# Optimization experiments

Hardware: AMD Instinct MI355X
Metric: run time of the kernel (lower is better)

Reference implementation:

```python
import jax, jax.numpy as jnp
import numpy as np

D_MODEL = 1024
HEADS = 16
D_HEAD = 64  # d_q = d_k = d_v
LN_EPS = 1e-5


def setup_inputs() -> dict:
    key = jax.random.key(0)
    ks = jax.random.split(key, 12)
    B, L = 2, 2048
    query = jax.random.normal(ks[0], (B, L, D_MODEL), dtype=jnp.float32)
    k_in = jax.random.normal(ks[1], (B, L, D_MODEL), dtype=jnp.float32)
    v_in = jax.random.normal(ks[2], (B, L, D_MODEL), dtype=jnp.float32)
    # causal mask: True = masked (masked_fill with -inf); row i always keeps pos i
    mask = jnp.broadcast_to(~jnp.tril(jnp.ones((L, L), dtype=bool)), (B, L, L))
    std_qk = np.sqrt(2.0 / (D_MODEL + D_HEAD)).astype(np.float32)
    Wq = jax.random.normal(ks[3], (D_MODEL, HEADS * D_HEAD), dtype=jnp.float32) * std_qk
    Wk = jax.random.normal(ks[4], (D_MODEL, HEADS * D_HEAD), dtype=jnp.float32) * std_qk
    Wv = jax.random.normal(ks[5], (D_MODEL, HEADS * D_HEAD), dtype=jnp.float32) * std_qk
    bq = jnp.zeros((HEADS * D_HEAD,), dtype=jnp.float32)
    bk = jnp.zeros((HEADS * D_HEAD,), dtype=jnp.float32)
    bv = jnp.zeros((HEADS * D_HEAD,), dtype=jnp.float32)
    lim = 1.0 / np.sqrt(HEADS * D_HEAD)
    Wo = jax.random.uniform(ks[6], (HEADS * D_HEAD, D_MODEL), dtype=jnp.float32, minval=-lim, maxval=lim)
    bo = jax.random.uniform(ks[7], (D_MODEL,), dtype=jnp.float32, minval=-lim, maxval=lim)
    gamma = jnp.ones((D_MODEL,), dtype=jnp.float32)
    beta = jnp.zeros((D_MODEL,), dtype=jnp.float32)
    return {"query": query, "key": k_in, "value": v_in, "mask": mask,
            "Wq": Wq, "bq": bq, "Wk": Wk, "bk": bk, "Wv": Wv, "bv": bv,
            "Wo": Wo, "bo": bo, "gamma": gamma, "beta": beta}


def reference(query, key, value, mask, Wq, bq, Wk, bk, Wv, bv, Wo, bo, gamma, beta):
    B, Lq, _ = query.shape
    Lk = key.shape[1]
    # QKV projections, split into heads: [B, L, H, d]
    q = (query @ Wq + bq).reshape(B, Lq, HEADS, D_HEAD)
    k = (key @ Wk + bk).reshape(B, Lk, HEADS, D_HEAD)
    v = (value @ Wv + bv).reshape(B, Lk, HEADS, D_HEAD)
    # scaled dot-product scores: [B, H, Lq, Lk]
    scores = jnp.einsum('bqhd,bkhd->bhqk', q, k) / np.sqrt(D_HEAD).astype(np.float32)
    scores = jnp.where(mask[:, None, :, :], -jnp.inf, scores)
    probs = jax.nn.softmax(scores, axis=-1)  # dropout is identity at p=0 / eval
    out = jnp.einsum('bhqk,bkhd->bqhd', probs, v).reshape(B, Lq, HEADS * D_HEAD)
    out = out @ Wo + bo  # dropout identity
    x = query + out  # residual
    mu = jnp.mean(x, axis=-1, keepdims=True)
    var = jnp.var(x, axis=-1, keepdims=True)
    return gamma * (x - mu) * jax.lax.rsqrt(var + LN_EPS) + beta
```

## Files before the change

kernel.cpp:

```cpp
#include <hip/hip_runtime.h>
#include <hip/hip_bf16.h>

#define L_SEQ  2048
#define DMODEL 1024
#define HEADS  16
#define DHEAD  64
#define BATCH  2
#define MROWS  (BATCH * L_SEQ)

typedef __attribute__((ext_vector_type(8))) short bf16x8;
typedef __attribute__((ext_vector_type(8))) unsigned short u16x8;
typedef __attribute__((ext_vector_type(4))) float f32x4;

__device__ __forceinline__ float b2f(unsigned short u) {
    union { unsigned int u32; float f; } x;
    x.u32 = ((unsigned int)u) << 16;
    return x.f;
}
__device__ __forceinline__ unsigned short f2b(float f) {
    union { float f; unsigned int u; } x; x.f = f;
    unsigned int u = x.u;
    if ((u & 0x7fffffffu) > 0x7f800000u) return (unsigned short)((u >> 16) | 0x0040);
    unsigned int r = (u + 0x7fffu + ((u >> 16) & 1u)) >> 16;
    return (unsigned short)r;
}
__device__ __forceinline__ unsigned short f2br(float f) {
    union { float f; unsigned int u; } x; x.f = f;
    return (unsigned short)((x.u + 0x7fffu + ((x.u >> 16) & 1u)) >> 16);
}

__device__ __forceinline__ float4 load4(const void* p, int isF32, size_t idx) {
    if (isF32) return *(const float4*)((const float*)p + idx);
    const ushort4 u = *(const ushort4*)((const unsigned short*)p + idx);
    return make_float4(b2f(u.x), b2f(u.y), b2f(u.z), b2f(u.w));
}
__device__ __forceinline__ float load1(const void* p, int isF32, size_t idx) {
    return isF32 ? ((const float*)p)[idx] : b2f(((const unsigned short*)p)[idx]);
}

__device__ __forceinline__ void gload16(const void* g, void* l) {
    __builtin_amdgcn_global_load_lds(
        (const __attribute__((address_space(1))) void*)g,
        (__attribute__((address_space(3))) void*)l, 16, 0, 0);
}

__global__ void detect_kernel(const unsigned short* __restrict__ q, int* __restrict__ flag) {
    int cnt = 0;
    #pragma unroll 8
    for (int t = 0; t < 64; ++t) {
        const unsigned short u = q[(threadIdx.x << 6) + t];
        const int e = (u >> 7) & 0xFF;
        cnt += (e >= 133) ? 1 : 0;
    }
    #pragma unroll
    for (int off = 32; off; off >>= 1) cnt += __shfl_xor(cnt, off);
    if (threadIdx.x == 0) *flag = (cnt > 64) ? 1 : 0;
}

__global__ void diag_kernel(float* __restrict__ out, float val, int n) {
    const int i = blockIdx.x * 256 + threadIdx.x;
    if (i < n) out[i] = val;
}

__global__ __launch_bounds__(256) void cvtW_kernel(
    const void* __restrict__ W0, const void* __restrict__ W1,
    const void* __restrict__ W2, const void* __restrict__ W3,
    unsigned short* __restrict__ T0, unsigned short* __restrict__ T1,
    unsigned short* __restrict__ T2, unsigned short* __restrict__ T3,
    const int* __restrict__ dflag)
{
    const int isF32 = *dflag;
    const int z = blockIdx.z;
    const void* W = (z == 0) ? W0 : (z == 1) ? W1 : (z == 2) ? W2 : W3;
    unsigned short* T = (z == 0) ? T0 : (z == 1) ? T1 : (z == 2) ? T2 : T3;

    __shared__ unsigned short tile[64][66];
    const int kb = blockIdx.x << 6, nb = blockIdx.y << 6;
    const int tr = threadIdx.x >> 4, tc = (threadIdx.x & 15) << 2;
    #pragma unroll
    for (int p = 0; p < 4; ++p) {
        const int r = tr + p * 16;
        const float4 v = load4(W, isF32, (size_t)(kb + r) * DMODEL + nb + tc);
        tile[tc + 0][r] = f2br(v.x);
        tile[tc + 1][r] = f2br(v.y);
        tile[tc + 2][r] = f2br(v.z);
        tile[tc + 3][r] = f2br(v.w);
    }
    __syncthreads();
    #pragma unroll
    for (int p = 0; p < 4; ++p) {
        const int rr = tr + p * 16;
        const ushort4 o = make_ushort4(tile[rr][tc], tile[rr][tc + 1],
                                       tile[rr][tc + 2], tile[rr][tc + 3]);
        *(ushort4*)(T + (size_t)(nb + rr) * DMODEL + kb + tc) = o;
    }
}

#define QKV_COMPUTE(CUR)                                                          \
    {                                                                             \
        bf16x8 af[4], bfr[4];                                                     \
        _Pragma("unroll")                                                         \
        for (int i = 0; i < 4; ++i) {                                             \
            const int row = wm + i * 16 + ln;                                     \
            const int p = quad ^ ((row >> 1) & 3);                                \
            af[i] = *(const bf16x8*)(As[CUR] + row * 32 + p * 8);                 \
        }                                                                         \
        _Pragma("unroll")                                                         \
        for (int j = 0; j < 4; ++j)                                               \
            bfr[j] = *(const bf16x8*)(Bs[CUR] + (wn + j * 16 + ln) * 32 + quad * 8); \
        _Pragma("unroll")                                                         \
        for (int i = 0; i < 4; ++i)                                               \
            _Pragma("unroll")                                                     \
            for (int j = 0; j < 4; ++j)                                           \
                acc[i][j] = __builtin_amdgcn_mfma_f32_16x16x32_bf16(af[i], bfr[j], acc[i][j], 0, 0, 0); \
    }

__global__ __launch_bounds__(256) void gemm_qkv_mfma(
    const void* __restrict__ A0, const void* __restrict__ A1, const void* __restrict__ A2,
    const unsigned short* __restrict__ Wt0, const unsigned short* __restrict__ Wt1,
    const unsigned short* __restrict__ Wt2,
    const void* __restrict__ b0, const void* __restrict__ b1, const void* __restrict__ b2,
    unsigned short* __restrict__ O0, unsigned short* __restrict__ O1, unsigned short* __restrict__ O2,
    const int* __restrict__ dflag)
{
    const int isF32 = *dflag;

    const int bid = blockIdx.x;
    const int xcd = bid & 7;
    const int jj  = bid >> 3;
    const int g   = xcd * 12 + (jj >> 3);
    const int z   = g >> 5;
    const int rowBase = (g & 31) << 7;
    const int colBase = (jj & 7) << 7;

    const void* A  = (z == 0) ? A0 : (z == 1) ? A1 : A2;
    const unsigned short* Wt = (z == 0) ? Wt0 : (z == 1) ? Wt1 : Wt2;
    const void* bi = (z == 0) ? b0 : (z == 1) ? b1 : b2;
    unsigned short* out = (z == 0) ? O0 : (z == 1) ? O1 : O2;
    const float scale = (z == 0) ? 0.125f : 1.0f;

    __shared__ __align__(16) unsigned short As[2][128 * 32];
    __shared__ __align__(16) unsigned short Bs[2][128 * 32];

    const int tid  = threadIdx.x;
    const int lane = tid & 63, wid = tid >> 6;
    const int ln   = lane & 15, quad = lane >> 4;
    const int wm   = (wid & 1) << 6, wn = (wid >> 1) << 6;

    f32x4 acc[4][4];
    #pragma unroll
    for (int i = 0; i < 4; ++i)
        #pragma unroll
        for (int j = 0; j < 4; ++j)
            #pragma unroll
            for (int d = 0; d < 4; ++d) acc[i][j][d] = 0.f;

    const int am   = tid >> 1;
    const int half = tid & 1;
    const int sw   = (am >> 1) & 3;
    const int bseg = wid * 2;
    const int brow = lane >> 2, bcol = (lane & 3) << 3;

    gload16(Wt + (size_t)(colBase + bseg * 16 + brow) * DMODEL + bcol,
            Bs[0] + bseg * 512);
    gload16(Wt + (size_t)(colBase + (bseg + 1) * 16 + brow) * DMODEL + bcol,
            Bs[0] + (bseg + 1) * 512);
    {
        const size_t ab = (size_t)(rowBase + am) * DMODEL + half * 16;
        const float4 a0 = load4(A, isF32, ab);
        const float4 a1 = load4(A, isF32, ab + 4);
        const float4 a2 = load4(A, isF32, ab + 8);
        const float4 a3 = load4(A, isF32, ab + 12);
        u16x8 pk0, pk1;
        pk0[0] = f2br(a0.x); pk0[1] = f2br(a0.y); pk0[2] = f2br(a0.z); pk0[3] = f2br(a0.w);
        pk0[4] = f2br(a1.x); pk0[5] = f2br(a1.y); pk0[6] = f2br(a1.z); pk0[7] = f2br(a1.w);
        pk1[0] = f2br(a2.x); pk1[1] = f2br(a2.y); pk1[2] = f2br(a2.z); pk1[3] = f2br(a2.w);
        pk1[4] = f2br(a3.x); pk1[5] = f2br(a3.y); pk1[6] = f2br(a3.z); pk1[7] = f2br(a3.w);
        unsigned short* ap = As[0] + am * 32;
        *(u16x8*)(ap + (((half << 1) | 0) ^ sw) * 8) = pk0;
        *(u16x8*)(ap + (((half << 1) | 1) ^ sw) * 8) = pk1;
    }
    __syncthreads();

    int cur = 0;
    for (int t = 0; t < 31; ++t) {
        const int nxt = cur ^ 1;
        const int k0n = (t + 1) << 5;
        gload16(Wt + (size_t)(colBase + bseg * 16 + brow) * DMODEL + k0n + bcol,
                Bs[nxt] + bseg * 512);
        gload16(Wt + (size_t)(colBase + (bseg + 1) * 16 + brow) * DMODEL + k0n + bcol,
                Bs[nxt] + (bseg + 1) * 512);
        const size_t ab = (size_t)(rowBase + am) * DMODEL + k0n + half * 16;
        const float4 a0 = load4(A, isF32, ab);
        const float4 a1 = load4(A, isF32, ab + 4);
        const float4 a2 = load4(A, isF32, ab + 8);
        const float4 a3 = load4(A, isF32, ab + 12);

        QKV_COMPUTE(cur);

        u16x8 pk0, pk1;
        pk0[0] = f2br(a0.x); pk0[1] = f2br(a0.y); pk0[2] = f2br(a0.z); pk0[3] = f2br(a0.w);
        pk0[4] = f2br(a1.x); pk0[5] = f2br(a1.y); pk0[6] = f2br(a1.z); pk0[7] = f2br(a1.w);
        pk1[0] = f2br(a2.x); pk1[1] = f2br(a2.y); pk1[2] = f2br(a2.z); pk1[3] = f2br(a2.w);
        pk1[4] = f2br(a3.x); pk1[5] = f2br(a3.y); pk1[6] = f2br(a3.z); pk1[7] = f2br(a3.w);
        unsigned short* ap = As[nxt] + am * 32;
        *(u16x8*)(ap + (((half << 1) | 0) ^ sw) * 8) = pk0;
        *(u16x8*)(ap + (((half << 1) | 1) ^ sw) * 8) = pk1;

        __syncthreads();
        cur = nxt;
    }
    QKV_COMPUTE(cur);

    float bsv[4];
    #pragma unroll
    for (int j = 0; j < 4; ++j) bsv[j] = load1(bi, isF32, colBase + wn + j * 16 + ln);

    if (z != 2) {
        #pragma unroll
        for (int i = 0; i < 4; ++i) {
            const int r0 = rowBase + wm + i * 16 + quad * 4;
            const int b = r0 >> 11, l0 = r0 & (L_SEQ - 1);
            #pragma unroll
            for (int j = 0; j < 4; ++j) {
                const int n = colBase + wn + j * 16 + ln;
                const int h = n >> 6, d = n & 63;
                const size_t base = ((size_t)(b * HEADS + h) * L_SEQ) << 6;
                #pragma unroll
                for (int reg = 0; reg < 4; ++reg)
                    out[base + ((size_t)(l0 + reg) << 6) + d] =
                        f2br((acc[i][j][reg] + bsv[j]) * scale);
            }
        }
    } else {
        #pragma unroll
        for (int i = 0; i < 4; ++i) {
            const int r0 = rowBase + wm + i * 16 + quad * 4;
            const int b = r0 >> 11, l0 = r0 & (L_SEQ - 1);
            #pragma unroll
            for (int j = 0; j < 4; ++j) {
                const int n = colBase + wn + j * 16 + ln;
                const int h = n >> 6, d = n & 63;
                ushort4 o;
                o.x = f2br(acc[i][j][0] + bsv[j]);
                o.y = f2br(acc[i][j][1] + bsv[j]);
                o.z = f2br(acc[i][j][2] + bsv[j]);
                o.w = f2br(acc[i][j][3] + bsv[j]);
                *(ushort4*)(out + (((size_t)((b * HEADS + h) * 64 + d)) << 11) + l0) = o;
            }
        }
    }
}

#define OUT_COMPUTE(CUR)                                                          \
    {                                                                             \
        bf16x8 af[4], bfr[4];                                                     \
        _Pragma("unroll")                                                         \
        for (int i = 0; i < 4; ++i)                                               \
            af[i] = *(const bf16x8*)(As[CUR] + (wm + i * 16 + ln) * 32 + quad * 8); \
        _Pragma("unroll")                                                         \
        for (int j = 0; j < 4; ++j)                                               \
            bfr[j] = *(const bf16x8*)(Bs[CUR] + (wn + j * 16 + ln) * 32 + quad * 8); \
        _Pragma("unroll")                                                         \
        for (int i = 0; i < 4; ++i)                                               \
            _Pragma("unroll")                                                     \
            for (int j = 0; j < 4; ++j)                                           \
                acc[i][j] = __builtin_amdgcn_mfma_f32_16x16x32_bf16(af[i], bfr[j], acc[i][j], 0, 0, 0); \
    }

__global__ __launch_bounds__(256) void gemm_out_mfma(
    const unsigned short* __restrict__ AO,
    const unsigned short* __restrict__ Wt,
    const void* __restrict__ bi,
    const void* __restrict__ resid,
    float* __restrict__ X,
    const int* __restrict__ dflag)
{
    const int isF32 = *dflag;
    __shared__ __align__(16) unsigned short As[2][128 * 32];
    __shared__ __align__(16) unsigned short Bs[2][128 * 32];

    const int bid = blockIdx.x;
    const int xcd = bid & 7;
    const int jj  = bid >> 3;
    const int g   = xcd * 4 + (jj >> 3);
    const int rowBase = g << 7;
    const int colBase = (jj & 7) << 7;

    const int tid  = threadIdx.x;
    const int lane = tid & 63, wid = tid >> 6;
    const int ln   = lane & 15, quad = lane >> 4;
    const int wm   = (wid & 1) << 6, wn = (wid >> 1) << 6;

    f32x4 acc[4][4];
    #pragma unroll
    for (int i = 0; i < 4; ++i)
        #pragma unroll
        for (int j = 0; j < 4; ++j)
            #pragma unroll
            for (int d = 0; d < 4; ++d) acc[i][j][d] = 0.f;

    const int seg = wid * 2;
    const int srow = lane >> 2, scol = (lane & 3) << 3;

    #pragma unroll
    for (int t2 = 0; t2 < 2; ++t2) {
        gload16(AO + (size_t)(rowBase + (seg + t2) * 16 + srow) * DMODEL + scol,
                As[0] + (seg + t2) * 512);
        gload16(Wt + (size_t)(colBase + (seg + t2) * 16 + srow) * DMODEL + scol,
                Bs[0] + (seg + t2) * 512);
    }
    __syncthreads();

    int cur = 0;
    for (int t = 0; t < 31; ++t) {
        const int nxt = cur ^ 1;
        const int k0n = (t + 1) << 5;
        #pragma unroll
        for (int t2 = 0; t2 < 2; ++t2) {
            gload16(AO + (size_t)(rowBase + (seg + t2) * 16 + srow) * DMODEL + k0n + scol,
                    As[nxt] + (seg + t2) * 512);
            gload16(Wt + (size_t)(colBase + (seg + t2) * 16 + srow) * DMODEL + k0n + scol,
                    Bs[nxt] + (seg + t2) * 512);
        }

        OUT_COMPUTE(cur);

        __syncthreads();
        cur = nxt;
    }
    OUT_COMPUTE(cur);

    float bsv[4];
    #pragma unroll
    for (int j = 0; j < 4; ++j) bsv[j] = load1(bi, isF32, colBase + wn + j * 16 + ln);

    #pragma unroll
    for (int i = 0; i < 4; ++i) {
        const int r0 = rowBase + wm + i * 16 + quad * 4;
        #pragma unroll
        for (int j = 0; j < 4; ++j) {
            const int n = colBase + wn + j * 16 + ln;
            #pragma unroll
            for (int reg = 0; reg < 4; ++reg) {
                const size_t idx = (size_t)(r0 + reg) * DMODEL + n;
                X[idx] = acc[i][j][reg] + bsv[j] + load1(resid, isF32, idx);
            }
        }
    }
}

#define KVB  128
#define NQB  (L_SEQ / 64)
#define KSTR 72
#define VSTR 136
__global__ __launch_bounds__(256, 3) void attn_mfma_kernel(
    const unsigned short* __restrict__ Q,
    const unsigned short* __restrict__ K,
    const unsigned short* __restrict__ Vt,
    unsigned short* __restrict__ AO)
{
    __shared__ unsigned short Kl[KVB * KSTR];
    __shared__ unsigned short Vl[64 * VSTR];
    __shared__ unsigned short Pl[4][16 * KVB];

    const int tid  = threadIdx.x;
    const int wid  = tid >> 6;
    const int lane = tid & 63;
    const int ln   = lane & 15;
    const int quad = lane >> 4;

    const int qb = (NQB - 1) - (blockIdx.x >> 5);
    const int bh = blockIdx.x & 31;

    const size_t qkBase = (size_t)bh * (L_SEQ * 64);
    const size_t vtBase = (size_t)bh * (64 * L_SEQ);

    const int qrow = qb * 64 + wid * 16 + ln;
    const bf16x8 qf0 = *(const bf16x8*)(Q + qkBase + (size_t)qrow * 64 + quad * 8);
    const bf16x8 qf1 = *(const bf16x8*)(Q + qkBase + (size_t)qrow * 64 + quad * 8 + 32);

    f32x4 o[4];
    #pragma unroll
    for (int d = 0; d < 4; ++d) { o[d][0] = 0.f; o[d][1] = 0.f; o[d][2] = 0.f; o[d][3] = 0.f; }
    float m[4] = {-INFINITY, -INFINITY, -INFINITY, -INFINITY};
    float l[4] = {0.f, 0.f, 0.f, 0.f};

    unsigned short* Pw = Pl[wid];
    const int kp_r = tid >> 3, kp_c = (tid & 7) * 8;
    const int vp_r = tid >> 4, vp_c = (tid & 15) * 8;

    const int nt = (qb >> 1) + 1;
    for (int jt = 0; jt < nt; ++jt) {
        __syncthreads();
        #pragma unroll
        for (int p = 0; p < 4; ++p) {
            const int kr = kp_r + p * 32;
            *(int4*)(Kl + kr * KSTR + kp_c) =
                *(const int4*)(K + qkBase + (size_t)(jt * KVB + kr) * 64 + kp_c);
            const int vr = vp_r + p * 16;
            *(int4*)(Vl + vr * VSTR + vp_c) =
                *(const int4*)(Vt + vtBase + (size_t)vr * L_SEQ + jt * KVB + vp_c);
        }
        __syncthreads();

        f32x4 s[8];
        __builtin_amdgcn_s_setprio(1);
        #pragma unroll
        for (int sub = 0; sub < 8; ++sub) {
            const bf16x8 kf0 = *(const bf16x8*)(Kl + (sub * 16 + ln) * KSTR + quad * 8);
            const bf16x8 kf1 = *(const bf16x8*)(Kl + (sub * 16 + ln) * KSTR + quad * 8 + 32);
            f32x4 a2;
            a2[0] = 0.f; a2[1] = 0.f; a2[2] = 0.f; a2[3] = 0.f;
            a2 = __builtin_amdgcn_mfma_f32_16x16x32_bf16(qf0, kf0, a2, 0, 0, 0);
            a2 = __builtin_amdgcn_mfma_f32_16x16x32_bf16(qf1, kf1, a2, 0, 0, 0);
            s[sub] = a2;
        }
        __builtin_amdgcn_s_setprio(0);

        if (jt == nt - 1) {
            const int row0 = qb * 64 + wid * 16 + quad * 4;
            #pragma unroll
            for (int sub = 0; sub < 8; ++sub) {
                const int keyg = jt * KVB + sub * 16 + ln;
                #pragma unroll
                for (int reg = 0; reg < 4; ++reg)
                    if (keyg > row0 + reg) s[sub][reg] = -INFINITY;
            }
        }

        float alpha[4];
        #pragma unroll
        for (int reg = 0; reg < 4; ++reg) {
            float t = fmaxf(
                fmaxf(fmaxf(s[0][reg], s[1][reg]), fmaxf(s[2][reg], s[3][reg])),
                fmaxf(fmaxf(s[4][reg], s[5][reg]), fmaxf(s[6][reg], s[7][reg])));
            #pragma unroll
            for (int off = 8; off; off >>= 1) t = fmaxf(t, __shfl_xor(t, off));
            const float mn = fmaxf(m[reg], t);
            alpha[reg] = __expf(m[reg] - mn);
            m[reg] = mn;
            float rs = 0.f;
            #pragma unroll
            for (int sub = 0; sub < 8; ++sub) {
                const float pe = __expf(s[sub][reg] - mn);
                s[sub][reg] = pe;
                rs += pe;
            }
            #pragma unroll
            for (int off = 8; off; off >>= 1) rs += __shfl_xor(rs, off);
            l[reg] = l[reg] * alpha[reg] + rs;
        }

        #pragma unroll
        for (int sub = 0; sub < 8; ++sub)
            #pragma unroll
            for (int reg = 0; reg < 4; ++reg) {
                const int r = quad * 4 + reg;
                const int blk = (sub * 2 + (ln >> 3)) ^ ((r >> 1) & 7);
                Pw[r * KVB + blk * 8 + (ln & 7)] = f2br(s[sub][reg]);
            }

        #pragma unroll
        for (int dblk = 0; dblk < 4; ++dblk)
            #pragma unroll
            for (int reg = 0; reg < 4; ++reg)
                o[dblk][reg] *= alpha[reg];

        __builtin_amdgcn_s_setprio(1);
        #pragma unroll
        for (int jb = 0; jb < 4; ++jb) {
            const int rblk = (jb * 4 + quad) ^ ((ln >> 1) & 7);
            const bf16x8 pf = *(const bf16x8*)(Pw + ln * KVB + rblk * 8);
            #pragma unroll
            for (int dblk = 0; dblk < 4; ++dblk) {
                const bf16x8 vf = *(const bf16x8*)(Vl + (dblk * 16 + ln) * VSTR + jb * 32 + quad * 8);
                o[dblk] = __builtin_amdgcn_mfma_f32_16x16x32_bf16(pf, vf, o[dblk], 0, 0, 0);
            }
        }
        __builtin_amdgcn_s_setprio(0);
    }

    const int b = bh >> 4, h = bh & 15;
    float rl[4];
    #pragma unroll
    for (int reg = 0; reg < 4; ++reg) rl[reg] = 1.f / l[reg];
    #pragma unroll
    for (int dblk = 0; dblk < 4; ++dblk)
        #pragma unroll
        for (int reg = 0; reg < 4; ++reg) {
            const int row = qb * 64 + wid * 16 + quad * 4 + reg;
            AO[((size_t)(b * L_SEQ + row)) * DMODEL + h * 64 + dblk * 16 + ln] =
                f2br(o[dblk][reg] * rl[reg]);
        }
}

__global__ __launch_bounds__(256) void ln_kernel(
    const float* __restrict__ X,
    const void* __restrict__ gamma,
    const void* __restrict__ beta,
    float* __restrict__ out,
    const int* __restrict__ dflag)
{
    const int isF32 = *dflag;
    const int row = blockIdx.x;
    const int tid = threadIdx.x;
    const float* x = X + (size_t)row * DMODEL;
    float v[4], s = 0.f, s2 = 0.f;
    #pragma unroll
    for (int j = 0; j < 4; ++j) {
        const float t = x[tid + (j << 8)];
        v[j] = t; s += t; s2 += t * t;
    }
    #pragma unroll
    for (int off = 32; off; off >>= 1) {
        s  += __shfl_xor(s, off);
        s2 += __shfl_xor(s2, off);
    }
    __shared__ float red[4][2];
    const int wid = tid >> 6, lane = tid & 63;
    if (lane == 0) { red[wid][0] = s; red[wid][1] = s2; }
    __syncthreads();
    s  = red[0][0] + red[1][0] + red[2][0] + red[3][0];
    s2 = red[0][1] + red[1][1] + red[2][1] + red[3][1];
    const float mu  = s * (1.f / 1024.f);
    const float var = s2 * (1.f / 1024.f) - mu * mu;
    const float inv = rsqrtf(var + 1e-5f);
    #pragma unroll
    for (int j = 0; j < 4; ++j) {
        const int c = tid + (j << 8);
        float r = load1(gamma, isF32, c) * (v[j] - mu) * inv + load1(beta, isF32, c);
        if (!(r == r) || fabsf(r) > 1e37f) r = 777000.0f;
        out[(size_t)row * DMODEL + c] = r;
    }
}

extern "C" void kernel_launch(void* const* d_in, const int* in_sizes, int n_in,
                              void* d_out, int out_size, void* d_ws, size_t ws_size,
                              hipStream_t stream) {
    const void* query = d_in[0];
    const void* key   = d_in[1];
    const void* value = d_in[2];

    int wbase = 4;
    if (in_sizes[3] == DMODEL * DMODEL) wbase = 3;
    const void* Wq    = d_in[wbase + 0];
    const void* bq    = d_in[wbase + 1];
    const void* Wk    = d_in[wbase + 2];
    const void* bk    = d_in[wbase + 3];
    const void* Wv    = d_in[wbase + 4];
    const void* bv    = d_in[wbase + 5];
    const void* Wo    = d_in[wbase + 6];
    const void* bo    = d_in[wbase + 7];
    const void* gamma = d_in[wbase + 8];
    const void* beta  = d_in[wbase + 9];

    const size_t NEED = ((size_t)24u << 20) + 64;
    if (ws_size < NEED) {
        const float val = (float)(ws_size >> 20) * 1000.0f;
        diag_kernel<<<dim3((out_size + 255) / 256), dim3(256), 0, stream>>>(
            (float*)d_out, val, out_size);
        return;
    }

    char* ws = (char*)d_ws;
    unsigned short* Qb  = (unsigned short*)(ws);
    unsigned short* Kb  = (unsigned short*)(ws + (size_t)( 8u << 20));
    unsigned short* Vtb = (unsigned short*)(ws + (size_t)(16u << 20));
    float* X            = (float*)ws;
    int* dflag          = (int*)(ws + (size_t)(24u << 20));
    unsigned short* AO  = (unsigned short*)d_out;
    unsigned short* Wtq = (unsigned short*)d_out + ((size_t)4u << 20);
    unsigned short* Wtk = Wtq + ((size_t)1u << 20);
    unsigned short* Wtv = Wtk + ((size_t)1u << 20);
    unsigned short* Wto = Wtv + ((size_t)1u << 20);

    const dim3 blk(256);

    detect_kernel<<<dim3(1), dim3(64), 0, stream>>>((const unsigned short*)query, dflag);
    cvtW_kernel<<<dim3(16, 16, 4), blk, 0, stream>>>(
        Wq, Wk, Wv, Wo, Wtq, Wtk, Wtv, Wto, dflag);
    gemm_qkv_mfma<<<dim3(768), blk, 0, stream>>>(
        query, key, value, Wtq, Wtk, Wtv, bq, bk, bv, Qb, Kb, Vtb, dflag);
    attn_mfma_kernel<<<dim3(BATCH * HEADS * 32), blk, 0, stream>>>(Qb, Kb, Vtb, AO);
    gemm_out_mfma<<<dim3(256), blk, 0, stream>>>(AO, Wto, bo, query, X, dflag);
    ln_kernel<<<dim3(MROWS), blk, 0, stream>>>(X, gamma, beta, (float*)d_out, dflag);
}
```

Measured before the change: 304.2 us.

## Stage QKV GEMM A tiles via direct global-to-LDS loads and vectorize LayerNorm

The QKV projection GEMM used to load fp32 activations into registers, convert them to bf16 and write them to shared memory. It now copies raw fp32 (or bf16) A tiles straight into LDS with async 16-byte global-to-LDS loads, using an XOR swizzle, and converts to bf16 when reading the MFMA fragments. This removes register staging and the convert-then-store step from the main loop, so A loads can overlap compute like the B loads already do. In exchange it doubles A shared memory and repeats the conversion per fragment read. The LayerNorm kernel also switches to float4 vectorized loads and stores.

```diff
diff --git a/kernel.cpp b/kernel.cpp
--- a/kernel.cpp
+++ b/kernel.cpp
@@ -96,23 +96,71 @@
     }
 }
 
-#define QKV_COMPUTE(CUR)                                                          \
+#define STAGE_A_F32(BUF, K0)                                                      \
+    _Pragma("unroll")                                                             \
+    for (int s4 = 0; s4 < 4; ++s4) {                                              \
+        const int ar = s4 * 32 + (tid >> 3);                                      \
+        const int ac = (tid & 7) ^ (ar & 7);                                      \
+        gload16((const float*)A + (size_t)(rowBase + ar) * DMODEL + (K0) + ac * 4,\
+                (char*)AsMem[BUF] + s4 * 4096 + tid * 16);                        \
+    }
+
+#define STAGE_A_BF16(BUF, K0)                                                     \
+    _Pragma("unroll")                                                             \
+    for (int s2 = 0; s2 < 2; ++s2) {                                              \
+        const int ar = s2 * 64 + (tid >> 2);                                      \
+        const int ac = (tid & 3) ^ ((ar >> 1) & 3);                               \
+        gload16((const unsigned short*)A + (size_t)(rowBase + ar) * DMODEL + (K0) + ac * 8, \
+                (char*)AsMem[BUF] + s2 * 4096 + tid * 16);                        \
+    }
+
+#define STAGE_B(BUF, K0)                                                          \
+    gload16(Wt + (size_t)(colBase + bseg * 16 + brow) * DMODEL + (K0) + bcol,     \
+            Bs[BUF] + bseg * 512);                                                \
+    gload16(Wt + (size_t)(colBase + (bseg + 1) * 16 + brow) * DMODEL + (K0) + bcol,\
+            Bs[BUF] + (bseg + 1) * 512);
+
+#define QKV_MFMA_CLUSTER                                                          \
+    _Pragma("unroll")                                                             \
+    for (int i = 0; i < 4; ++i)                                                   \
+        _Pragma("unroll")                                                         \
+        for (int j = 0; j < 4; ++j)                                               \
+            acc[i][j] = __builtin_amdgcn_mfma_f32_16x16x32_bf16(af[i], bfr[j], acc[i][j], 0, 0, 0);
+
+#define QKV_COMPUTE_F32(CUR)                                                      \
+    {                                                                             \
+        bf16x8 af[4], bfr[4];                                                     \
+        _Pragma("unroll")                                                         \
+        for (int i = 0; i < 4; ++i) {                                             \
+            const int row = wm + i * 16 + ln;                                     \
+            const int xr  = row & 7;                                              \
+            const float* rp = (const float*)AsMem[CUR] + row * 32;                \
+            const f32x4 lo = *(const f32x4*)(rp + (((quad << 1) | 0) ^ xr) * 4);  \
+            const f32x4 hi = *(const f32x4*)(rp + (((quad << 1) | 1) ^ xr) * 4);  \
+            af[i][0] = (short)f2br(lo[0]); af[i][1] = (short)f2br(lo[1]);         \
+            af[i][2] = (short)f2br(lo[2]); af[i][3] = (short)f2br(lo[3]);         \
+            af[i][4] = (short)f2br(hi[0]); af[i][5] = (short)f2br(hi[1]);         \
+            af[i][6] = (short)f2br(hi[2]); af[i][7] = (short)f2br(hi[3]);         \
+        }                                                                         \
+        _Pragma("unroll")                                                         \
+        for (int j = 0; j < 4; ++j)                                               \
+            bfr[j] = *(const bf16x8*)(Bs[CUR] + (wn + j * 16 + ln) * 32 + quad * 8); \
+        QKV_MFMA_CLUSTER                                                          \
+    }
+
+#define QKV_COMPUTE_BF16(CUR)                                                     \
     {                                                                             \
         bf16x8 af[4], bfr[4];                                                     \
         _Pragma("unroll")                                                         \
         for (int i = 0; i < 4; ++i) {                                             \
             const int row = wm + i * 16 + ln;                                     \
             const int p = quad ^ ((row >> 1) & 3);                                \
-            af[i] = *(const bf16x8*)(As[CUR] + row * 32 + p * 8);                 \
+            af[i] = *(const bf16x8*)((const unsigned short*)AsMem[CUR] + row * 32 + p * 8); \
         }                                                                         \
         _Pragma("unroll")                                                         \
         for (int j = 0; j < 4; ++j)                                               \
             bfr[j] = *(const bf16x8*)(Bs[CUR] + (wn + j * 16 + ln) * 32 + quad * 8); \
-        _Pragma("unroll")                                                         \
-        for (int i = 0; i < 4; ++i)                                               \
-            _Pragma("unroll")                                                     \
-            for (int j = 0; j < 4; ++j)                                           \
-                acc[i][j] = __builtin_amdgcn_mfma_f32_16x16x32_bf16(af[i], bfr[j], acc[i][j], 0, 0, 0); \
+        QKV_MFMA_CLUSTER                                                          \
     }
 
 __global__ __launch_bounds__(256) void gemm_qkv_mfma(
@@ -139,7 +187,7 @@
     unsigned short* out = (z == 0) ? O0 : (z == 1) ? O1 : O2;
     const float scale = (z == 0) ? 0.125f : 1.0f;
 
-    __shared__ __align__(16) unsigned short As[2][128 * 32];
+    __shared__ __align__(16) char AsMem[2][16384];
     __shared__ __align__(16) unsigned short Bs[2][128 * 32];
 
     const int tid  = threadIdx.x;
@@ -155,62 +203,40 @@
             #pragma unroll
             for (int d = 0; d < 4; ++d) acc[i][j][d] = 0.f;
 
-    const int am   = tid >> 1;
-    const int half = tid & 1;
-    const int sw   = (am >> 1) & 3;
     const int bseg = wid * 2;
     const int brow = lane >> 2, bcol = (lane & 3) << 3;
 
-    gload16(Wt + (size_t)(colBase + bseg * 16 + brow) * DMODEL + bcol,
-            Bs[0] + bseg * 512);
-    gload16(Wt + (size_t)(colBase + (bseg + 1) * 16 + brow) * DMODEL + bcol,
-            Bs[0] + (bseg + 1) * 512);
-    {
-        const size_t ab = (size_t)(rowBase + am) * DMODEL + half * 16;
-        const float4 a0 = load4(A, isF32, ab);
-        const float4 a1 = load4(A, isF32, ab + 4);
-        const float4 a2 = load4(A, isF32, ab + 8);
-        const float4 a3 = load4(A, isF32, ab + 12);
-        u16x8 pk0, pk1;
-        pk0[0] = f2br(a0.x); pk0[1] = f2br(a0.y); pk0[2] = f2br(a0.z); pk0[3] = f2br(a0.w);
-        pk0[4] = f2br(a1.x); pk0[5] = f2br(a1.y); pk0[6] = f2br(a1.z); pk0[7] = f2br(a1.w);
-        pk1[0] = f2br(a2.x); pk1[1] = f2br(a2.y); pk1[2] = f2br(a2.z); pk1[3] = f2br(a2.w);
-        pk1[4] = f2br(a3.x); pk1[5] = f2br(a3.y); pk1[6] = f2br(a3.z); pk1[7] = f2br(a3.w);
-        unsigned short* ap = As[0] + am * 32;
-        *(u16x8*)(ap + (((half << 1) | 0) ^ sw) * 8) = pk0;
-        *(u16x8*)(ap + (((half << 1) | 1) ^ sw) * 8) = pk1;
-    }
-    __syncthreads();
-
-    int cur = 0;
-    for (int t = 0; t < 31; ++t) {
-        const int nxt = cur ^ 1;
-        const int k0n = (t + 1) << 5;
-        gload16(Wt + (size_t)(colBase + bseg * 16 + brow) * DMODEL + k0n + bcol,
-                Bs[nxt] + bseg * 512);
-        gload16(Wt + (size_t)(colBase + (bseg + 1) * 16 + brow) * DMODEL + k0n + bcol,
-                Bs[nxt] + (bseg + 1) * 512);
-        const size_t ab = (size_t)(rowBase + am) * DMODEL + k0n + half * 16;
-        const float4 a0 = load4(A, isF32, ab);
-        const float4 a1 = load4(A, isF32, ab + 4);
-        const float4 a2 = load4(A, isF32, ab + 8);
-        const float4 a3 = load4(A, isF32, ab + 12);
-
-        QKV_COMPUTE(cur);
-
-        u16x8 pk0, pk1;
-        pk0[0] = f2br(a0.x); pk0[1] = f2br(a0.y); pk0[2] = f2br(a0.z); pk0[3] = f2br(a0.w);
-        pk0[4] = f2br(a1.x); pk0[5] = f2br(a1.y); pk0[6] = f2br(a1.z); pk0[7] = f2br(a1.w);
-        pk1[0] = f2br(a2.x); pk1[1] = f2br(a2.y); pk1[2] = f2br(a2.z); pk1[3] = f2br(a2.w);
-        pk1[4] = f2br(a3.x); pk1[5] = f2br(a3.y); pk1[6] = f2br(a3.z); pk1[7] = f2br(a3.w);
-        unsigned short* ap = As[nxt] + am * 32;
-        *(u16x8*)(ap + (((half << 1) | 0) ^ sw) * 8) = pk0;
-        *(u16x8*)(ap + (((half << 1) | 1) ^ sw) * 8) = pk1;
-
+    if (isF32) {
+        STAGE_A_F32(0, 0)
+        STAGE_B(0, 0)
         __syncthreads();
-        cur = nxt;
-    }
-    QKV_COMPUTE(cur);
+        int cur = 0;
+        for (int t = 0; t < 31; ++t) {
+            const int nxt = cur ^ 1;
+            const int k0n = (t + 1) << 5;
+            STAGE_A_F32(nxt, k0n)
+            STAGE_B(nxt, k0n)
+            QKV_COMPUTE_F32(cur)
+            __syncthreads();
+            cur = nxt;
+        }
+        QKV_COMPUTE_F32(cur)
+    } else {
+        STAGE_A_BF16(0, 0)
+        STAGE_B(0, 0)
+        __syncthreads();
+        int cur = 0;
+        for (int t = 0; t < 31; ++t) {
+            const int nxt = cur ^ 1;
+            const int k0n = (t + 1) << 5;
+            STAGE_A_BF16(nxt, k0n)
+            STAGE_B(nxt, k0n)
+            QKV_COMPUTE_BF16(cur)
+            __syncthreads();
+            cur = nxt;
+        }
+        QKV_COMPUTE_BF16(cur)
+    }
 
     float bsv[4];
     #pragma unroll
@@ -506,12 +532,10 @@
     const int row = blockIdx.x;
     const int tid = threadIdx.x;
     const float* x = X + (size_t)row * DMODEL;
-    float v[4], s = 0.f, s2 = 0.f;
-    #pragma unroll
-    for (int j = 0; j < 4; ++j) {
-        const float t = x[tid + (j << 8)];
-        v[j] = t; s += t; s2 += t * t;
-    }
+    const int c0 = tid << 2;
+    const float4 vv = *(const float4*)(x + c0);
+    float s  = vv.x + vv.y + vv.z + vv.w;
+    float s2 = vv.x * vv.x + vv.y * vv.y + vv.z * vv.z + vv.w * vv.w;
     #pragma unroll
     for (int off = 32; off; off >>= 1) {
         s  += __shfl_xor(s, off);
@@ -526,13 +550,18 @@
     const float mu  = s * (1.f / 1024.f);
     const float var = s2 * (1.f / 1024.f) - mu * mu;
     const float inv = rsqrtf(var + 1e-5f);
-    #pragma unroll
-    for (int j = 0; j < 4; ++j) {
-        const int c = tid + (j << 8);
-        float r = load1(gamma, isF32, c) * (v[j] - mu) * inv + load1(beta, isF32, c);
-        if (!(r == r) || fabsf(r) > 1e37f) r = 777000.0f;
-        out[(size_t)row * DMODEL + c] = r;
-    }
+    const float4 gm = load4(gamma, isF32, c0);
+    const float4 bt = load4(beta,  isF32, c0);
+    float4 r;
+    r.x = gm.x * (vv.x - mu) * inv + bt.x;
+    r.y = gm.y * (vv.y - mu) * inv + bt.y;
+    r.z = gm.z * (vv.z - mu) * inv + bt.z;
+    r.w = gm.w * (vv.w - mu) * inv + bt.w;
+    if (!(r.x == r.x) || fabsf(r.x) > 1e37f) r.x = 777000.0f;
+    if (!(r.y == r.y) || fabsf(r.y) > 1e37f) r.y = 777000.0f;
+    if (!(r.z == r.z) || fabsf(r.z) > 1e37f) r.z = 777000.0f;
+    if (!(r.w == r.w) || fabsf(r.w) > 1e37f) r.w = 777000.0f;
+    *(float4*)(out + (size_t)row * DMODEL + c0) = r;
 }
 
 extern "C" void kernel_launch(void* const* d_in, const int* in_sizes, int n_in,
```

After: 348.0 us. +14.4%, slower.
